# Performance work log

Measured on AMD Instinct MI355X. Metric: run time of the kernel, lower is better.

The kernel has to match this reference:

```python
import jax, jax.numpy as jnp
import numpy as np

EMBED = 1024
ATTN = 1024
HEADS = 16
HEAD_DIM = ATTN // HEADS


def setup_inputs() -> dict:
    key = jax.random.key(0)
    ks = jax.random.split(key, 8)
    s = 1.0 / np.sqrt(EMBED)
    sa = 1.0 / np.sqrt(ATTN)
    return {
        "queries": jax.random.normal(ks[0], (4, 512, EMBED), jnp.float32),
        "context": jax.random.normal(ks[1], (4, 2048, EMBED), jnp.float32),
        "Wq": jax.random.normal(ks[2], (EMBED, ATTN), jnp.float32) * s,
        "bq": jnp.zeros((ATTN,), jnp.float32),
        "Wkv": jax.random.normal(ks[3], (EMBED, 2 * ATTN), jnp.float32) * s,
        "bkv": jnp.zeros((2 * ATTN,), jnp.float32),
        "Wo": jax.random.normal(ks[4], (ATTN, EMBED), jnp.float32) * sa,
        "bo": jnp.zeros((EMBED,), jnp.float32),
    }


def reference(queries, context, Wq, bq, Wkv, bkv, Wo, bo):
    B, Lq, _ = queries.shape
    Lk = context.shape[1]
    q = queries @ Wq + bq                      # [B, Lq, ATTN]
    kv = context @ Wkv + bkv                   # [B, Lk, 2*ATTN]
    k, v = jnp.split(kv, 2, axis=-1)
    q = q.reshape(B, Lq, HEADS, HEAD_DIM)
    k = k.reshape(B, Lk, HEADS, HEAD_DIM)
    v = v.reshape(B, Lk, HEADS, HEAD_DIM)
    scale = 1.0 / np.sqrt(HEAD_DIM)
    scores = jnp.einsum("bqhd,bkhd->bhqk", q, k) * scale
    attn = jax.nn.softmax(scores, axis=-1)
    x = jnp.einsum("bhqk,bkhd->bqhd", attn, v).reshape(B, Lq, ATTN)
    return x @ Wo + bo
```

## Files before the change

kernel.cpp:

```cpp
#include <hip/hip_runtime.h>
#include <hip/hip_bf16.h>
#include <stdint.h>

typedef unsigned short u16;
typedef __attribute__((ext_vector_type(8))) __bf16 bf16x8;
typedef __attribute__((ext_vector_type(2))) __bf16 bf16x2;
typedef __attribute__((ext_vector_type(4))) float f32x4;
typedef __attribute__((ext_vector_type(4))) u16 u16x4;
typedef __attribute__((ext_vector_type(4))) float f32x4v;

typedef __attribute__((address_space(1))) void gvoid_t;
typedef __attribute__((address_space(3))) void lvoid_t;

#define BAR()    asm volatile("s_barrier" ::: "memory")
#define WAITV0() asm volatile("s_waitcnt vmcnt(0)" ::: "memory")
#define WAITV2() asm volatile("s_waitcnt vmcnt(2)" ::: "memory")
#define WAITV4() asm volatile("s_waitcnt vmcnt(4)" ::: "memory")
#define WAITV8() asm volatile("s_waitcnt vmcnt(8)" ::: "memory")

__device__ inline u16 f2bf(float f) {
    uint32_t u = __float_as_uint(f);
    u += 0x7fff + ((u >> 16) & 1);
    return (u16)(u >> 16);
}

__device__ inline float bf2f(u16 v) {
    return __uint_as_float(((uint32_t)v) << 16);
}

__device__ inline void gll16(const void* g, void* l) {
    __builtin_amdgcn_global_load_lds((gvoid_t*)g, (lvoid_t*)l, 16, 0, 0);
}

__device__ inline f32x4 mfma16(bf16x8 a, bf16x8 b, f32x4 c) {
    return __builtin_amdgcn_mfma_f32_16x16x32_bf16(a, b, c, 0, 0, 0);
}

__device__ inline int vslot(int r) {
    int n = r >> 4;
    return ((n >> 1) << 5) + (((r >> 2) & 3) << 3) + ((n & 1) << 2) + (r & 3);
}

__global__ __launch_bounds__(256) void prep_kernel(
        const float* __restrict__ q, const float* __restrict__ c,
        const float* __restrict__ Wq, const float* __restrict__ Wkv,
        const float* __restrict__ Wo, u16* __restrict__ qb,
        u16* __restrict__ cb, u16* __restrict__ WqT,
        u16* __restrict__ WkvT, u16* __restrict__ WoT) {
    const int bid = blockIdx.x;
    const int tid = threadIdx.x;
    if (bid < 10240) {
        int i = bid * 256 + tid;
        const float* src; u16* dst; int j;
        if (i < 524288) { src = q; dst = qb; j = i; }
        else            { src = c; dst = cb; j = i - 524288; }
        f32x4v f = ((const f32x4v*)src)[j];
        u16x4 o;
        o[0] = f2bf(f[0]); o[1] = f2bf(f[1]); o[2] = f2bf(f[2]); o[3] = f2bf(f[3]);
        ((u16x4*)dst)[j] = o;
        return;
    }
    int b2 = bid - 10240;
    const float* W; u16* WT; int N, n0, k0;
    if (b2 < 1024)      { W = Wq;  WT = WqT;  N = 1024; n0 = (b2 & 31) * 32; k0 = (b2 >> 5) * 32; }
    else if (b2 < 3072) { int b3 = b2 - 1024; W = Wkv; WT = WkvT; N = 2048; n0 = (b3 & 63) * 32; k0 = (b3 >> 6) * 32; }
    else                { int b3 = b2 - 3072; W = Wo;  WT = WoT;  N = 1024; n0 = (b3 & 31) * 32; k0 = (b3 >> 5) * 32; }
    __shared__ float t[32][33];
    int x = tid & 31, y = tid >> 5;
    for (int yy = y; yy < 32; yy += 8)
        t[yy][x] = W[(size_t)(k0 + yy) * N + n0 + x];
    __syncthreads();
    for (int yy = y; yy < 32; yy += 8)
        WT[(size_t)(n0 + yy) * 1024 + k0 + x] = f2bf(t[x][yy]);
}

template <int MODE>
__global__ __launch_bounds__(512, 2) void gemm_bt(
        const u16* __restrict__ A, const u16* __restrict__ Bt,
        const float* __restrict__ bias, int M, int N, int K,
        float scale, void* __restrict__ out0) {
    __shared__ u16 lds[4][6144];
    const int NT = K >> 5;
    const int tid = threadIdx.x;
    const int lane = tid & 63, wv = tid >> 6;
    const int c16 = lane & 15, g = lane >> 4;
    const int m0 = blockIdx.y * 64, n0 = blockIdx.x * 128;

    const int idxA = (wv & 3) * 64 + lane;
    const int rA = idxA >> 2, ccA = (idxA & 3) ^ ((rA >> 1) & 3);
    const size_t offA = (size_t)(m0 + rA) * K + ccA * 8;
    const int dstA = (wv & 3) * 512;
    const int idxB = wv * 64 + lane;
    const int rB = idxB >> 2, ccB = (idxB & 3) ^ ((rB >> 1) & 3);
    const size_t offB = (size_t)(n0 + rB) * K + ccB * 8;
    const int dstB = 2048 + wv * 512;

    auto stage = [&](int t) {
        gll16(A + offA + t * 32, &lds[t & 3][dstA]);
        gll16(Bt + offB + t * 32, &lds[t & 3][dstB]);
    };

    const int wm = (wv >> 1) * 16, wn = (wv & 1) * 64;
    f32x4 acc[4] = {};

    auto compute = [&](int slot) {
        const u16* la = &lds[slot][0];
        const u16* lb = &lds[slot][2048];
        int rowa = wm + c16;
        bf16x8 af = *(const bf16x8*)&la[rowa * 32 + (g ^ ((rowa >> 1) & 3)) * 8];
        bf16x8 bfr[4];
#pragma unroll
        for (int n = 0; n < 4; n++) {
            int row = wn + n * 16 + c16;
            bfr[n] = *(const bf16x8*)&lb[row * 32 + (g ^ ((row >> 1) & 3)) * 8];
        }
#pragma unroll
        for (int n = 0; n < 4; n++)
            acc[n] = mfma16(af, bfr[n], acc[n]);
    };

    stage(0); stage(1); stage(2);

    for (int t = 0; t < NT - 2; ++t) {
        WAITV4();
        BAR();
        if (t + 3 < NT) stage(t + 3);
        compute(t & 3);
    }
    WAITV2(); BAR(); compute((NT - 2) & 3);
    WAITV0(); BAR(); compute((NT - 1) & 3);

#pragma unroll
    for (int n = 0; n < 4; n++) {
        int col = n0 + wn + n * 16 + c16;
        float bv = bias[col];
        int rowb = m0 + wm + g * 4;
#pragma unroll
        for (int j = 0; j < 4; j++) {
            float v = (acc[n][j] + bv) * scale;
            int row = rowb + j;
            if (MODE == 0) {
                ((u16*)out0)[(size_t)row * N + col] = f2bf(v);
            } else {
                ((float*)out0)[(size_t)row * N + col] = v;
            }
        }
    }
}

__global__ __launch_bounds__(512, 2) void fused_qkv(
        const u16* __restrict__ cb, const u16* __restrict__ WkvT,
        const float* __restrict__ bkv, u16* __restrict__ Kp,
        u16* __restrict__ VpT,
        const u16* __restrict__ qb, const u16* __restrict__ WqT,
        const float* __restrict__ bq, float qscale, u16* __restrict__ Qp) {
    __shared__ u16 smem[4][2][8192];
    const int tid = threadIdx.x;
    const int lane = tid & 63, wv = tid >> 6;
    const int c16 = lane & 15, g = lane >> 4;
    const int bidg = blockIdx.x;

    if (bidg < 256) {
        const int K = 1024, NT = 32;
        const int cpx = 32;
        const int sw = (bidg & 7) * cpx + (bidg >> 3);
        const int bx = sw & 7, by = sw >> 3;
        const int m0 = by * 256, n0 = bx * 256;

        const int isB = wv >> 2;
        const int rbase = (wv & 3) * 64;
        const u16* src = isB ? WkvT : cb;
        const int base0 = isB ? n0 : m0;
        size_t off[4];
        const u16* ldst[4];
#pragma unroll
        for (int i = 0; i < 4; i++) {
            int rl = rbase + i * 16 + (lane >> 2);
            int ch = (lane & 3) ^ ((rl >> 1) & 3);
            off[i] = (size_t)(base0 + rl) * K + ch * 8;
            ldst[i] = &smem[0][0][0] + ((size_t)isB * 256 * 32) + (size_t)(rbase + i * 16) * 32;
        }
        const size_t slotStride = 2 * 256 * 32;

        auto stage = [&](int t) {
            const u16* s0 = src + (size_t)t * 32;
            u16* d = (u16*)ldst[0] + (size_t)(t & 3) * slotStride;
            gll16(s0 + off[0], d);
            gll16(s0 + off[1], d + 16 * 32);
            gll16(s0 + off[2], d + 32 * 32);
            gll16(s0 + off[3], d + 48 * 32);
        };

        const int wm = wv >> 2;
        const int wn = wv & 3;
        f32x4 acc[8][4] = {};

        auto compute = [&](int slot) {
            const u16* la = &smem[slot][0][0];
            const u16* lb = &smem[slot][1][0];
            bf16x8 af[8], bfr[4];
#pragma unroll
            for (int m = 0; m < 8; m++) {
                int row = wm * 128 + m * 16 + c16;
                af[m] = *(const bf16x8*)&la[row * 32 + (g ^ ((row >> 1) & 3)) * 8];
            }
#pragma unroll
            for (int n = 0; n < 4; n++) {
                int row = wn * 64 + n * 16 + c16;
                bfr[n] = *(const bf16x8*)&lb[row * 32 + (g ^ ((row >> 1) & 3)) * 8];
            }
#pragma unroll
            for (int m = 0; m < 8; m++)
#pragma unroll
                for (int n = 0; n < 4; n++)
                    acc[m][n] = mfma16(af[m], bfr[n], acc[m][n]);
        };

        stage(0); stage(1); stage(2);

        for (int t = 0; t < NT - 2; ++t) {
            WAITV8();
            BAR();
            if (t + 3 < NT) stage(t + 3);
            compute(t & 3);
        }
        WAITV4(); BAR(); compute((NT - 2) & 3);
        WAITV0(); BAR(); compute((NT - 1) & 3);

        const bool isV = (n0 >= 1024);
#pragma unroll
        for (int n = 0; n < 4; n++) {
            int col = n0 + wn * 64 + n * 16 + c16;
            float bv = bkv[col];
#pragma unroll
            for (int m = 0; m < 8; m++) {
                int rowb = m0 + wm * 128 + m * 16 + g * 4;
                if (isV) {
                    u16x4 pk;
#pragma unroll
                    for (int j = 0; j < 4; j++) pk[j] = f2bf(acc[m][n][j] + bv);
                    int vcol = (rowb & ~63) + vslot(rowb & 63);
                    *(u16x4*)&VpT[(size_t)(col - 1024) * 8192 + vcol] = pk;
                } else {
#pragma unroll
                    for (int j = 0; j < 4; j++)
                        Kp[(size_t)(rowb + j) * 1024 + col] = f2bf(acc[m][n][j] + bv);
                }
            }
        }
    } else {
        const int K = 1024, N = 1024, NT = 32;
        const int b2 = bidg - 256;
        const int m0 = (b2 >> 3) * 64, n0 = (b2 & 7) * 128;
        u16* base = &smem[0][0][0];

        const int idxA = (wv & 3) * 64 + lane;
        const int rA = idxA >> 2, ccA = (idxA & 3) ^ ((rA >> 1) & 3);
        const size_t offA = (size_t)(m0 + rA) * K + ccA * 8;
        const int dstA = (wv & 3) * 512;
        const int idxB = wv * 64 + lane;
        const int rB = idxB >> 2, ccB = (idxB & 3) ^ ((rB >> 1) & 3);
        const size_t offB = (size_t)(n0 + rB) * K + ccB * 8;
        const int dstB = 2048 + wv * 512;

        auto stage = [&](int t) {
            u16* d = base + (t & 3) * 6144;
            gll16(qb + offA + t * 32, d + dstA);
            gll16(WqT + offB + t * 32, d + dstB);
        };

        const int wm = (wv >> 1) * 16, wn = (wv & 1) * 64;
        f32x4 acc[4] = {};

        auto compute = [&](int slot) {
            const u16* la = base + slot * 6144;
            const u16* lb = la + 2048;
            int rowa = wm + c16;
            bf16x8 af = *(const bf16x8*)&la[rowa * 32 + (g ^ ((rowa >> 1) & 3)) * 8];
            bf16x8 bfr[4];
#pragma unroll
            for (int n = 0; n < 4; n++) {
                int row = wn + n * 16 + c16;
                bfr[n] = *(const bf16x8*)&lb[row * 32 + (g ^ ((row >> 1) & 3)) * 8];
            }
#pragma unroll
            for (int n = 0; n < 4; n++)
                acc[n] = mfma16(af, bfr[n], acc[n]);
        };

        stage(0); stage(1); stage(2);

        for (int t = 0; t < NT - 2; ++t) {
            WAITV4();
            BAR();
            if (t + 3 < NT) stage(t + 3);
            compute(t & 3);
        }
        WAITV2(); BAR(); compute((NT - 2) & 3);
        WAITV0(); BAR(); compute((NT - 1) & 3);

#pragma unroll
        for (int n = 0; n < 4; n++) {
            int col = n0 + wn + n * 16 + c16;
            float bv = bq[col];
            int rowb = m0 + wm + g * 4;
#pragma unroll
            for (int j = 0; j < 4; j++) {
                float v = (acc[n][j] + bv) * qscale;
                Qp[(size_t)(rowb + j) * N + col] = f2bf(v);
            }
        }
    }
}

__global__ __launch_bounds__(256, 3) void attn_split_kernel(
        const u16* __restrict__ Qp, const u16* __restrict__ Kp,
        const u16* __restrict__ VpT, u16* __restrict__ Opart,
        float* __restrict__ ml) {
    __shared__ u16 lKV[3][2][64 * 64];
    const int NT = 16;
    const int tid = threadIdx.x;
    const int lane = tid & 63, wv = tid >> 6;
    const int c16 = lane & 15, g = lane >> 4;
    const int bid = blockIdx.x;
    const int qblk = bid >> 7;
    const int low = bid & 127;
    const int h = low & 15, z = low >> 4;
    const int b = z >> 1, sp = z & 1;
    const int kvbase = sp * 1024;

    bf16x8 qf[2][2];
#pragma unroll
    for (int qs = 0; qs < 2; qs++) {
        int qrow = b * 512 + qblk * 128 + qs * 64 + wv * 16 + c16;
        qf[qs][0] = *(const bf16x8*)(Qp + (size_t)qrow * 1024 + h * 64 + g * 8);
        qf[qs][1] = *(const bf16x8*)(Qp + (size_t)qrow * 1024 + h * 64 + 32 + g * 8);
    }

    f32x4 acc[2][4] = {};
    float m_s[2] = {-1e30f, -1e30f}, l_s[2] = {0.f, 0.f};

    const int r0 = tid >> 3, c0 = (tid & 7) ^ (r0 & 7);
    const int r1 = 32 + r0,  c1 = (tid & 7) ^ (r1 & 7);
    const int dst0 = wv * 512, dst1 = 2048 + wv * 512;

    auto stageKV = [&](int t) {
        int slot = t % 3;
        int kv0 = kvbase + t * 64;
        u16* dK = &lKV[slot][0][0];
        u16* dV = &lKV[slot][1][0];
        gll16(Kp + (size_t)(b * 2048 + kv0 + r0) * 1024 + h * 64 + c0 * 8, dK + dst0);
        gll16(Kp + (size_t)(b * 2048 + kv0 + r1) * 1024 + h * 64 + c1 * 8, dK + dst1);
        gll16(VpT + (size_t)(h * 64 + r0) * 8192 + b * 2048 + kv0 + c0 * 8, dV + dst0);
        gll16(VpT + (size_t)(h * 64 + r1) * 8192 + b * 2048 + kv0 + c1 * 8, dV + dst1);
    };

    stageKV(0); stageKV(1);
    for (int t = 0; t < NT; ++t) {
        if (t < NT - 1) { WAITV4(); } else { WAITV0(); }
        BAR();
        if (t + 2 < NT) stageKV(t + 2);

        const int slot = t % 3;
        const u16* lK = &lKV[slot][0][0];
        const u16* lV = &lKV[slot][1][0];

        f32x4 s[2][4];
#pragma unroll
        for (int n = 0; n < 4; n++) {
            s[0][n] = f32x4{0.f, 0.f, 0.f, 0.f};
            s[1][n] = f32x4{0.f, 0.f, 0.f, 0.f};
        }
        __builtin_amdgcn_s_setprio(1);
#pragma unroll
        for (int n = 0; n < 4; n++) {
            int key = n * 16 + c16;
#pragma unroll
            for (int kk = 0; kk < 2; kk++) {
                bf16x8 kf = *(const bf16x8*)&lK[key * 64 + (((kk * 4 + g) ^ (key & 7))) * 8];
                s[0][n] = mfma16(kf, qf[0][kk], s[0][n]);
                s[1][n] = mfma16(kf, qf[1][kk], s[1][n]);
            }
        }
        __builtin_amdgcn_s_setprio(0);

        uint32_t r[2][4][2];
#pragma unroll
        for (int qs = 0; qs < 2; qs++) {
            float mn0 = fmaxf(fmaxf(s[qs][0][0], s[qs][0][1]), fmaxf(s[qs][0][2], s[qs][0][3]));
            float mn1 = fmaxf(fmaxf(s[qs][1][0], s[qs][1][1]), fmaxf(s[qs][1][2], s[qs][1][3]));
            float mn2 = fmaxf(fmaxf(s[qs][2][0], s[qs][2][1]), fmaxf(s[qs][2][2], s[qs][2][3]));
            float mn3 = fmaxf(fmaxf(s[qs][3][0], s[qs][3][1]), fmaxf(s[qs][3][2], s[qs][3][3]));
            float mx = fmaxf(fmaxf(mn0, mn1), fmaxf(mn2, mn3));
            mx = fmaxf(mx, __shfl_xor(mx, 16));
            mx = fmaxf(mx, __shfl_xor(mx, 32));

            if (!__all(mx - m_s[qs] <= 8.0f)) {
                float mn = fmaxf(m_s[qs], mx);
                float al = exp2f(m_s[qs] - mn);
                m_s[qs] = mn;
                l_s[qs] *= al;
                float alr[4];
#pragma unroll
                for (int j = 0; j < 4; j++) alr[j] = __shfl(al, g * 4 + j);
#pragma unroll
                for (int nd = 0; nd < 4; nd++)
#pragma unroll
                    for (int j = 0; j < 4; j++) acc[qs][nd][j] *= alr[j];
            }

            float sums[4];
#pragma unroll
            for (int n = 0; n < 4; n++) {
                float p0 = exp2f(s[qs][n][0] - m_s[qs]);
                float p1 = exp2f(s[qs][n][1] - m_s[qs]);
                float p2 = exp2f(s[qs][n][2] - m_s[qs]);
                float p3 = exp2f(s[qs][n][3] - m_s[qs]);
                sums[n] = (p0 + p1) + (p2 + p3);
                union { bf16x2 h; uint32_t u; } ca, cb;
                ca.h[0] = (__bf16)p0; ca.h[1] = (__bf16)p1;
                cb.h[0] = (__bf16)p2; cb.h[1] = (__bf16)p3;
                r[qs][n][0] = ca.u; r[qs][n][1] = cb.u;
            }
            float sum = (sums[0] + sums[1]) + (sums[2] + sums[3]);
            sum += __shfl_xor(sum, 16);
            sum += __shfl_xor(sum, 32);
            l_s[qs] += sum;
        }

        __builtin_amdgcn_s_setprio(1);
#pragma unroll
        for (int kk2 = 0; kk2 < 2; kk2++) {
            union { bf16x8 v8; uint32_t u[4]; } pa0, pa1;
            pa0.u[0] = r[0][kk2 * 2][0];     pa0.u[1] = r[0][kk2 * 2][1];
            pa0.u[2] = r[0][kk2 * 2 + 1][0]; pa0.u[3] = r[0][kk2 * 2 + 1][1];
            pa1.u[0] = r[1][kk2 * 2][0];     pa1.u[1] = r[1][kk2 * 2][1];
            pa1.u[2] = r[1][kk2 * 2 + 1][0]; pa1.u[3] = r[1][kk2 * 2 + 1][1];
#pragma unroll
            for (int nd = 0; nd < 4; nd++) {
                int d = nd * 16 + c16;
                bf16x8 vf = *(const bf16x8*)&lV[d * 64 + (((kk2 * 4 + g) ^ (d & 7))) * 8];
                acc[0][nd] = mfma16(pa0.v8, vf, acc[0][nd]);
                acc[1][nd] = mfma16(pa1.v8, vf, acc[1][nd]);
            }
        }
        __builtin_amdgcn_s_setprio(0);
    }

#pragma unroll
    for (int qs = 0; qs < 2; qs++) {
#pragma unroll
        for (int j = 0; j < 4; j++) {
            int rowq = b * 512 + qblk * 128 + qs * 64 + wv * 16 + g * 4 + j;
            size_t idx = (size_t)sp * 32768 + (size_t)rowq * 16 + h;
#pragma unroll
            for (int nd = 0; nd < 4; nd++)
                Opart[idx * 64 + nd * 16 + c16] = f2bf(acc[qs][nd][j]);
        }
        if (g == 0) {
            int rowq = b * 512 + qblk * 128 + qs * 64 + wv * 16 + c16;
            size_t idx = (size_t)sp * 32768 + (size_t)rowq * 16 + h;
            ml[idx * 2] = m_s[qs];
            ml[idx * 2 + 1] = l_s[qs];
        }
    }
}

__global__ __launch_bounds__(256) void attn_combine_kernel(
        const u16* __restrict__ Opart, const float* __restrict__ ml,
        u16* __restrict__ X) {
    const int tid = threadIdx.x;
    const int r = blockIdx.x * 4 + (tid >> 6);
    const int d = tid & 63;
    float m0 = ml[(size_t)r * 2], l0 = ml[(size_t)r * 2 + 1];
    float m1 = ml[(size_t)(32768 + r) * 2], l1 = ml[(size_t)(32768 + r) * 2 + 1];
    float M = fmaxf(m0, m1);
    float a0 = exp2f(m0 - M), a1 = exp2f(m1 - M);
    float li = 1.f / (l0 * a0 + l1 * a1);
    float o0 = bf2f(Opart[(size_t)r * 64 + d]);
    float o1 = bf2f(Opart[(size_t)(32768 + r) * 64 + d]);
    float o = (o0 * a0 + o1 * a1) * li;
    int qrow = r >> 4, h = r & 15;
    X[(size_t)qrow * 1024 + h * 64 + d] = f2bf(o);
}

extern "C" void kernel_launch(void* const* d_in, const int* in_sizes, int n_in,
                              void* d_out, int out_size, void* d_ws, size_t ws_size,
                              hipStream_t stream) {
    const float* queries = (const float*)d_in[0];
    const float* context = (const float*)d_in[1];
    const float* Wq      = (const float*)d_in[2];
    const float* bq      = (const float*)d_in[3];
    const float* Wkv     = (const float*)d_in[4];
    const float* bkv     = (const float*)d_in[5];
    const float* Wo      = (const float*)d_in[6];
    const float* bo      = (const float*)d_in[7];

    char* ws = (char*)d_ws;
    u16* qb   = (u16*)(ws);
    u16* cb   = (u16*)(ws + (4ull  << 20));
    u16* WqT  = (u16*)(ws + (20ull << 20));
    u16* WkvT = (u16*)(ws + (22ull << 20));
    u16* WoT  = (u16*)(ws + (26ull << 20));
    u16* Qp   = (u16*)(ws + (28ull << 20));
    u16* Kp   = (u16*)(ws + (32ull << 20));
    u16* VpT  = (u16*)(ws + (48ull << 20));
    u16* X    = (u16*)(ws + (64ull << 20));
    float* ml    = (float*)qb;
    u16*   Opart = (u16*)cb;

    prep_kernel<<<dim3(14336), dim3(256), 0, stream>>>(queries, context, Wq, Wkv, Wo,
                                                       qb, cb, WqT, WkvT, WoT);

    fused_qkv<<<dim3(512), dim3(512), 0, stream>>>(cb, WkvT, bkv, Kp, VpT,
                                                   qb, WqT, bq, 0.18033688f, Qp);
    attn_split_kernel<<<dim3(512), dim3(256), 0, stream>>>(Qp, Kp, VpT, Opart, ml);
    attn_combine_kernel<<<dim3(8192), dim3(256), 0, stream>>>(Opart, ml, X);
    gemm_bt<2><<<dim3(8, 32), dim3(512), 0, stream>>>(X, WoT, bo, 2048, 1024, 1024,
                                                      1.0f, d_out);
}
```

Before: 117.1 us.

## Fuse split-KV combine into attention kernel via atomic last-block reduction

Removes the separate attention combine kernel launch. Each split block publishes its partial output and max/sum stats, then bumps an atomic counter per (query block, batch, head) pair, and the second block to arrive merges its own register accumulator with the other split's partial and writes X directly. The counters are zeroed by an extra block in the prep kernel. This drops one launch and one read pass over its own half of the partial data, at the cost of thread fences, an atomic, and an uneven tail where only half the blocks do combine work.

```diff
diff --git a/kernel.cpp b/kernel.cpp
--- a/kernel.cpp
+++ b/kernel.cpp
@@ -46,9 +46,14 @@
         const float* __restrict__ Wq, const float* __restrict__ Wkv,
         const float* __restrict__ Wo, u16* __restrict__ qb,
         u16* __restrict__ cb, u16* __restrict__ WqT,
-        u16* __restrict__ WkvT, u16* __restrict__ WoT) {
+        u16* __restrict__ WkvT, u16* __restrict__ WoT,
+        uint32_t* __restrict__ cnt) {
     const int bid = blockIdx.x;
     const int tid = threadIdx.x;
+    if (bid == 14336) {
+        if (tid < 256) cnt[tid] = 0;
+        return;
+    }
     if (bid < 10240) {
         int i = bid * 256 + tid;
         const float* src; u16* dst; int j;
@@ -316,8 +321,10 @@
 __global__ __launch_bounds__(256, 3) void attn_split_kernel(
         const u16* __restrict__ Qp, const u16* __restrict__ Kp,
         const u16* __restrict__ VpT, u16* __restrict__ Opart,
-        float* __restrict__ ml) {
+        float* __restrict__ ml, uint32_t* __restrict__ cnt,
+        u16* __restrict__ X) {
     __shared__ u16 lKV[3][2][64 * 64];
+    __shared__ uint32_t sOld;
     const int NT = 16;
     const int tid = threadIdx.x;
     const int lane = tid & 63, wv = tid >> 6;
@@ -328,6 +335,7 @@
     const int h = low & 15, z = low >> 4;
     const int b = z >> 1, sp = z & 1;
     const int kvbase = sp * 1024;
+    const int pid = ((bid >> 5) << 4) | (bid & 15);
 
     bf16x8 qf[2][2];
 #pragma unroll
@@ -417,10 +425,10 @@
                 float p2 = exp2f(s[qs][n][2] - m_s[qs]);
                 float p3 = exp2f(s[qs][n][3] - m_s[qs]);
                 sums[n] = (p0 + p1) + (p2 + p3);
-                union { bf16x2 h; uint32_t u; } ca, cb;
-                ca.h[0] = (__bf16)p0; ca.h[1] = (__bf16)p1;
-                cb.h[0] = (__bf16)p2; cb.h[1] = (__bf16)p3;
-                r[qs][n][0] = ca.u; r[qs][n][1] = cb.u;
+                union { bf16x2 hh; uint32_t u; } ca, cb2;
+                ca.hh[0] = (__bf16)p0; ca.hh[1] = (__bf16)p1;
+                cb2.hh[0] = (__bf16)p2; cb2.hh[1] = (__bf16)p3;
+                r[qs][n][0] = ca.u; r[qs][n][1] = cb2.u;
             }
             float sum = (sums[0] + sums[1]) + (sums[2] + sums[3]);
             sum += __shfl_xor(sum, 16);
@@ -464,24 +472,39 @@
             ml[idx * 2 + 1] = l_s[qs];
         }
     }
-}
-
-__global__ __launch_bounds__(256) void attn_combine_kernel(
-        const u16* __restrict__ Opart, const float* __restrict__ ml,
-        u16* __restrict__ X) {
-    const int tid = threadIdx.x;
-    const int r = blockIdx.x * 4 + (tid >> 6);
-    const int d = tid & 63;
-    float m0 = ml[(size_t)r * 2], l0 = ml[(size_t)r * 2 + 1];
-    float m1 = ml[(size_t)(32768 + r) * 2], l1 = ml[(size_t)(32768 + r) * 2 + 1];
-    float M = fmaxf(m0, m1);
-    float a0 = exp2f(m0 - M), a1 = exp2f(m1 - M);
-    float li = 1.f / (l0 * a0 + l1 * a1);
-    float o0 = bf2f(Opart[(size_t)r * 64 + d]);
-    float o1 = bf2f(Opart[(size_t)(32768 + r) * 64 + d]);
-    float o = (o0 * a0 + o1 * a1) * li;
-    int qrow = r >> 4, h = r & 15;
-    X[(size_t)qrow * 1024 + h * 64 + d] = f2bf(o);
+
+    __threadfence();
+    __syncthreads();
+    if (tid == 0) sOld = atomicAdd(&cnt[pid], 1u);
+    __syncthreads();
+    if (sOld == 0) return;
+    __threadfence();
+
+    const int osp = sp ^ 1;
+#pragma unroll
+    for (int qs = 0; qs < 2; qs++) {
+        float mo[4], lo[4];
+#pragma unroll
+        for (int j = 0; j < 4; j++) {
+            mo[j] = __shfl(m_s[qs], g * 4 + j);
+            lo[j] = __shfl(l_s[qs], g * 4 + j);
+        }
+#pragma unroll
+        for (int j = 0; j < 4; j++) {
+            int rowq = b * 512 + qblk * 128 + qs * 64 + wv * 16 + g * 4 + j;
+            size_t idx = (size_t)osp * 32768 + (size_t)rowq * 16 + h;
+            float m1 = ml[idx * 2], l1 = ml[idx * 2 + 1];
+            float M = fmaxf(mo[j], m1);
+            float a0 = exp2f(mo[j] - M), a1 = exp2f(m1 - M);
+            float li = 1.f / (lo[j] * a0 + l1 * a1);
+#pragma unroll
+            for (int nd = 0; nd < 4; nd++) {
+                float o1 = bf2f(Opart[idx * 64 + nd * 16 + c16]);
+                float o = (acc[qs][nd][j] * a0 + o1 * a1) * li;
+                X[(size_t)rowq * 1024 + h * 64 + nd * 16 + c16] = f2bf(o);
+            }
+        }
+    }
 }
 
 extern "C" void kernel_launch(void* const* d_in, const int* in_sizes, int n_in,
@@ -506,16 +529,17 @@
     u16* Kp   = (u16*)(ws + (32ull << 20));
     u16* VpT  = (u16*)(ws + (48ull << 20));
     u16* X    = (u16*)(ws + (64ull << 20));
+    uint32_t* cnt = (uint32_t*)(ws + (68ull << 20));
     float* ml    = (float*)qb;
     u16*   Opart = (u16*)cb;
 
-    prep_kernel<<<dim3(14336), dim3(256), 0, stream>>>(queries, context, Wq, Wkv, Wo,
-                                                       qb, cb, WqT, WkvT, WoT);
+    prep_kernel<<<dim3(14337), dim3(256), 0, stream>>>(queries, context, Wq, Wkv, Wo,
+                                                       qb, cb, WqT, WkvT, WoT, cnt);
 
     fused_qkv<<<dim3(512), dim3(512), 0, stream>>>(cb, WkvT, bkv, Kp, VpT,
                                                    qb, WqT, bq, 0.18033688f, Qp);
-    attn_split_kernel<<<dim3(512), dim3(256), 0, stream>>>(Qp, Kp, VpT, Opart, ml);
-    attn_combine_kernel<<<dim3(8192), dim3(256), 0, stream>>>(Opart, ml, X);
+    attn_split_kernel<<<dim3(512), dim3(256), 0, stream>>>(Qp, Kp, VpT, Opart, ml,
+                                                           cnt, X);
     gemm_bt<2><<<dim3(8, 32), dim3(512), 0, stream>>>(X, WoT, bo, 2048, 1024, 1024,
                                                       1.0f, d_out);
 }
```

Result: slower. 200.6 us (+71.3%).
